# Kernel optimization log

Measured on AMD Instinct MI355X. Metric: run time of the kernel, lower is better.

## Reference

```python
import jax, jax.numpy as jnp
import numpy as np

QI8_MIN, QI8_MAX = -128.0, 127.0   # torch.qint8 iinfo
QU8_MIN, QU8_MAX = 0.0, 255.0      # torch.quint8 iinfo


def _assym_scale_offset(v, qmin, qmax):
    # mirrors get_tensor_assym_scale_offset: scale=(max-min)/(qmax-qmin), offset=qmin - min/scale
    vmin = v.min()
    vmax = v.max()
    scale = (vmax - vmin) / (qmax - qmin)
    offset = qmin - vmin / scale
    return scale, offset


def _fake_quant(v, scale, zp, qmin, qmax):
    # torch.quantize_per_tensor: q = clamp(round(v/scale + zp), qmin, qmax); dequant = (q - zp)*scale
    q = jnp.clip(jnp.round(v / scale + zp), qmin, qmax)
    return (q - zp) * scale


def setup_inputs() -> dict:
    key = jax.random.key(0)
    k1, k2, k3 = jax.random.split(key, 3)
    x = jax.random.normal(k1, (8192, 4096), jnp.float32)          # quantized activation input (modeled as float)
    weight = jax.random.normal(k2, (4096, 4096), jnp.float32) * 0.02  # Linear.weight [out, in]
    bias = jax.random.normal(k3, (4096,), jnp.float32) * 0.01
    return {"x": x, "weight": weight, "bias": bias}


def reference(x, weight, bias):
    # --- weight quantization (qint8, per-tensor asymmetric, done at __init__) ---
    w_scale, w_off = _assym_scale_offset(weight, QI8_MIN, QI8_MAX)
    w_zp = jnp.round(w_off)  # torch casts zero_point to int
    w_dq = _fake_quant(weight, w_scale, w_zp, QI8_MIN, QI8_MAX)

    # --- input is a quint8 quantized tensor; model quantize->dequantize ---
    x_scale, x_off = _assym_scale_offset(x, QU8_MIN, QU8_MAX)
    x_zp = jnp.round(x_off)
    x_dq = _fake_quant(x, x_scale, x_zp, QU8_MIN, QU8_MAX)

    # --- calibration pass (not _computed): float Linear on dequantized input ---
    act = x_dq @ weight.T + bias                 # [tokens, out]
    a_scale, a_off = _assym_scale_offset(act, QU8_MIN, QU8_MAX)
    a_zp = jnp.round(a_off)

    # --- qF.linear: int8 GEMM (dequantized form) + bias, requantized to quint8 ---
    out = x_dq @ w_dq.T + bias
    return _fake_quant(out, a_scale, a_zp, QU8_MIN, QU8_MAX)
```

## Files before the change

kernel.cpp:

```cpp
#include <hip/hip_runtime.h>
#include <stdint.h>

#define M_DIM 8192
#define N_DIM 4096
#define K_DIM 4096

typedef __attribute__((ext_vector_type(4))) int i32x4;

__device__ __forceinline__ unsigned fkey(float f) {
  unsigned u = __float_as_uint(f);
  return (u & 0x80000000u) ? ~u : (u | 0x80000000u);
}
__device__ __forceinline__ float finv(unsigned k) {
  return __uint_as_float((k & 0x80000000u) ? (k ^ 0x80000000u) : ~k);
}
__device__ __forceinline__ void async16(const void* g, void* l) {
  __builtin_amdgcn_global_load_lds(
      (const __attribute__((address_space(1))) void*)g,
      (__attribute__((address_space(3))) void*)l, 16, 0, 0);
}

__global__ void minmax_fused(const float* __restrict__ x, const float* __restrict__ w,
                             unsigned* __restrict__ stats) {
  const bool isX = blockIdx.x < 2048;
  const float4* v4 = isX ? (const float4*)x : (const float4*)w;
  const int n4 = isX ? (M_DIM * K_DIM / 4) : (N_DIM * K_DIM / 4);
  const int bid = isX ? blockIdx.x : (blockIdx.x - 2048);
  const int nb = isX ? 2048 : 1024;
  int i0 = bid * blockDim.x + threadIdx.x;
  int stride = nb * blockDim.x;
  float vmin = 3.4e38f, vmax = -3.4e38f;
  for (int i = i0; i < n4; i += stride) {
    float4 t = v4[i];
    vmin = fminf(vmin, fminf(fminf(t.x, t.y), fminf(t.z, t.w)));
    vmax = fmaxf(vmax, fmaxf(fmaxf(t.x, t.y), fmaxf(t.z, t.w)));
  }
  unsigned kmin = fkey(vmin), kmax = ~fkey(vmax);
  #pragma unroll
  for (int off = 32; off; off >>= 1) {
    unsigned t0 = __shfl_down(kmin, (unsigned)off, 64);
    unsigned t1 = __shfl_down(kmax, (unsigned)off, 64);
    kmin = kmin < t0 ? kmin : t0;
    kmax = kmax < t1 ? kmax : t1;
  }
  if ((threadIdx.x & 63) == 0) {
    int base = isX ? 0 : 2;
    atomicMin(&stats[base + 0], kmin);
    atomicMin(&stats[base + 1], kmax);
  }
}

__global__ void quant_fused(const float* __restrict__ x, const float* __restrict__ w,
                            const unsigned* __restrict__ stats,
                            signed char* __restrict__ A8, signed char* __restrict__ B8,
                            signed char* __restrict__ R8,
                            int* __restrict__ rowA, int* __restrict__ colB, int* __restrict__ colR) {
  __shared__ int sr[8];
  const int tid = threadIdx.x;
  const int lane = tid & 63;
  const int wv = tid >> 6;
  if (blockIdx.x < M_DIM) {
    const int row = blockIdx.x;
    const float xmin = finv(stats[0]), xmax = finv(~stats[1]);
    const float xs = (xmax - xmin) / 255.0f;
    const float xzp = rintf(0.0f - xmin / xs);
    const float4* xr = (const float4*)(x + (size_t)row * K_DIM);
    char4* ar = (char4*)(A8 + (size_t)row * K_DIM);
    int s = 0;
    #pragma unroll
    for (int i = 0; i < 4; ++i) {
      int idx = tid + i * 256;
      float4 t = xr[idx];
      int q0 = (int)(fminf(fmaxf(rintf(t.x / xs + xzp), 0.f), 255.f)) - 128;
      int q1 = (int)(fminf(fmaxf(rintf(t.y / xs + xzp), 0.f), 255.f)) - 128;
      int q2 = (int)(fminf(fmaxf(rintf(t.z / xs + xzp), 0.f), 255.f)) - 128;
      int q3 = (int)(fminf(fmaxf(rintf(t.w / xs + xzp), 0.f), 255.f)) - 128;
      char4 c4; c4.x = (signed char)q0; c4.y = (signed char)q1;
      c4.z = (signed char)q2; c4.w = (signed char)q3;
      ar[idx] = c4;
      s += q0 + q1 + q2 + q3;
    }
    #pragma unroll
    for (int off = 32; off; off >>= 1) s += __shfl_down(s, (unsigned)off, 64);
    if (lane == 0) sr[wv] = s;
    __syncthreads();
    if (tid == 0) rowA[row] = sr[0] + sr[1] + sr[2] + sr[3];
  } else {
    const int row = blockIdx.x - M_DIM;
    const float wmin = finv(stats[2]), wmax = finv(~stats[3]);
    const float ws = (wmax - wmin) / 255.0f;
    const float wzp = rintf(-128.0f - wmin / ws);
    const float inv_rs = 126.0f / ws;
    const float4* wr = (const float4*)(w + (size_t)row * K_DIM);
    char4* br = (char4*)(B8 + (size_t)row * K_DIM);
    char4* rr = (char4*)(R8 + (size_t)row * K_DIM);
    int sb = 0, srr = 0;
    #pragma unroll
    for (int i = 0; i < 4; ++i) {
      int idx = tid + i * 256;
      float4 t = wr[idx];
      char4 bq, rq;
      float v, qf; int q, r;
      v = t.x; qf = fminf(fmaxf(rintf(v / ws + wzp), -128.f), 127.f); q = (int)qf;
      r = (int)fminf(fmaxf(rintf((v - ws * (qf - wzp)) * inv_rs), -127.f), 127.f);
      bq.x = (signed char)q; rq.x = (signed char)r; sb += q; srr += r;
      v = t.y; qf = fminf(fmaxf(rintf(v / ws + wzp), -128.f), 127.f); q = (int)qf;
      r = (int)fminf(fmaxf(rintf((v - ws * (qf - wzp)) * inv_rs), -127.f), 127.f);
      bq.y = (signed char)q; rq.y = (signed char)r; sb += q; srr += r;
      v = t.z; qf = fminf(fmaxf(rintf(v / ws + wzp), -128.f), 127.f); q = (int)qf;
      r = (int)fminf(fmaxf(rintf((v - ws * (qf - wzp)) * inv_rs), -127.f), 127.f);
      bq.z = (signed char)q; rq.z = (signed char)r; sb += q; srr += r;
      v = t.w; qf = fminf(fmaxf(rintf(v / ws + wzp), -128.f), 127.f); q = (int)qf;
      r = (int)fminf(fmaxf(rintf((v - ws * (qf - wzp)) * inv_rs), -127.f), 127.f);
      bq.w = (signed char)q; rq.w = (signed char)r; sb += q; srr += r;
      br[idx] = bq; rr[idx] = rq;
    }
    #pragma unroll
    for (int off = 32; off; off >>= 1) {
      sb += __shfl_down(sb, (unsigned)off, 64);
      srr += __shfl_down(srr, (unsigned)off, 64);
    }
    if (lane == 0) { sr[wv] = sb; sr[4 + wv] = srr; }
    __syncthreads();
    if (tid == 0) {
      colB[row] = sr[0] + sr[1] + sr[2] + sr[3];
      colR[row] = sr[4] + sr[5] + sr[6] + sr[7];
    }
  }
}

__global__ __launch_bounds__(512, 4) void gemm_i8(
    const signed char* __restrict__ A8, const signed char* __restrict__ B8,
    const signed char* __restrict__ R8,
    const int* __restrict__ rowA, const int* __restrict__ colB, const int* __restrict__ colR,
    const float* __restrict__ bias, unsigned* __restrict__ stats,
    float* __restrict__ outp) {
  __shared__ __align__(16) signed char sA[3 * 128 * 64];
  __shared__ __align__(16) signed char sB[3 * 128 * 64];
  __shared__ __align__(16) signed char sR[3 * 128 * 64];
  __shared__ unsigned s_red[2];

  const int tid = threadIdx.x;
  const int wave = tid >> 6;
  const int lane = tid & 63;
  const int xcd = blockIdx.x & 7;
  const int s = blockIdx.x >> 3;
  const int bn = xcd * 4 + (s >> 6);
  const int bm = s & 63;
  const int rowBase = bm * 128;
  const int colBase = bn * 128;
  const int wr = wave >> 2;
  const int wc = wave & 3;
  const int laneR = lane & 15;
  const int laneK = (lane >> 4) * 16;

  if (tid == 0) { s_red[0] = 0xFFFFFFFFu; s_red[1] = 0xFFFFFFFFu; }

  i32x4 acc_q[4][2];
  i32x4 acc_r[4][2];
  const i32x4 zero = {0, 0, 0, 0};
  #pragma unroll
  for (int i = 0; i < 4; ++i) { acc_q[i][0] = zero; acc_q[i][1] = zero;
                                acc_r[i][0] = zero; acc_r[i][1] = zero; }

  const signed char* srcA = A8 + (size_t)(rowBase + wave * 16 + laneR) * K_DIM + laneK;
  const signed char* srcB = B8 + (size_t)(colBase + wave * 16 + laneR) * K_DIM + laneK;
  const signed char* srcR = R8 + (size_t)(colBase + wave * 16 + laneR) * K_DIM + laneK;
  signed char* dA = sA + wave * 1024 + lane * 16;
  signed char* dB = sB + wave * 1024 + lane * 16;
  signed char* dR = sR + wave * 1024 + lane * 16;

#define STAGE(off, kt) do {                      \
    async16(srcA + (kt), dA + (off));            \
    async16(srcB + (kt), dB + (off));            \
    async16(srcR + (kt), dR + (off));            \
  } while (0)

#define COMPUTE(off) do {                                                      \
    i32x4 af[4];                                                               \
    _Pragma("unroll")                                                          \
    for (int mi = 0; mi < 4; ++mi)                                             \
      af[mi] = *(const i32x4*)(sA + (off) + (wr * 4 + mi) * 1024 + lane * 16); \
    i32x4 bf[2], rf[2];                                                        \
    _Pragma("unroll")                                                          \
    for (int ni = 0; ni < 2; ++ni) {                                           \
      const int bo = (off) + (wc * 2 + ni) * 1024 + lane * 16;                 \
      bf[ni] = *(const i32x4*)(sB + bo);                                       \
      rf[ni] = *(const i32x4*)(sR + bo);                                       \
    }                                                                          \
    __builtin_amdgcn_s_setprio(1);                                             \
    _Pragma("unroll")                                                          \
    for (int ni = 0; ni < 2; ++ni) {                                           \
      _Pragma("unroll")                                                        \
      for (int mi = 0; mi < 4; ++mi) {                                         \
        acc_q[mi][ni] = __builtin_amdgcn_mfma_i32_16x16x64_i8(af[mi], bf[ni], acc_q[mi][ni], 0, 0, 0); \
        acc_r[mi][ni] = __builtin_amdgcn_mfma_i32_16x16x64_i8(af[mi], rf[ni], acc_r[mi][ni], 0, 0, 0); \
      }                                                                        \
    }                                                                          \
    __builtin_amdgcn_s_setprio(0);                                             \
  } while (0)

  STAGE(0, 0);
  STAGE(8192, 64);

  int o0 = 0, o1 = 8192, o2 = 16384;

  for (int t = 0; t < 62; ++t) {
    asm volatile("s_waitcnt vmcnt(3)" ::: "memory");
    __builtin_amdgcn_s_barrier();
    STAGE(o2, (t + 2) * 64);
    COMPUTE(o0);
    int tmp = o0; o0 = o1; o1 = o2; o2 = tmp;
  }
  asm volatile("s_waitcnt vmcnt(3)" ::: "memory");
  __builtin_amdgcn_s_barrier();
  COMPUTE(o0);
  { int tmp = o0; o0 = o1; o1 = o2; o2 = tmp; }
  asm volatile("s_waitcnt vmcnt(0)" ::: "memory");
  __builtin_amdgcn_s_barrier();
  COMPUTE(o0);

#undef STAGE
#undef COMPUTE

  const float xmin = finv(stats[0]), xmax = finv(~stats[1]);
  const float xs = (xmax - xmin) / 255.0f;
  const float xzp = rintf(0.0f - xmin / xs);
  const float wmin = finv(stats[2]), wmax = finv(~stats[3]);
  const float ws = (wmax - wmin) / 255.0f;
  const float wzp = rintf(-128.0f - wmin / ws);
  const int c = 128 - (int)xzp;
  const int wzpi = (int)wzp;
  const float sw = xs * ws;
  const float xrs = xs * (ws / 126.0f);
  const int ccK = c * wzpi * K_DIM;
  unsigned kmin = 0xFFFFFFFFu, kmax = 0xFFFFFFFFu;

  int rAv[4][4];
  #pragma unroll
  for (int mi = 0; mi < 4; ++mi) {
    const int row0 = rowBase + wr * 64 + mi * 16 + (lane >> 4) * 4;
    #pragma unroll
    for (int r = 0; r < 4; ++r) rAv[mi][r] = rowA[row0 + r];
  }

  #pragma unroll
  for (int ni = 0; ni < 2; ++ni) {
    const int col = colBase + wc * 32 + ni * 16 + laneR;
    const float bv = bias[col];
    const int base_n = c * colB[col] - ccK;
    const int cR = c * colR[col];
    #pragma unroll
    for (int mi = 0; mi < 4; ++mi) {
      const int row0 = rowBase + wr * 64 + mi * 16 + (lane >> 4) * 4;
      #pragma unroll
      for (int r = 0; r < 4; ++r) {
        const int S = acc_q[mi][ni][r] + base_n - wzpi * rAv[mi][r];
        const float ov = sw * (float)S + bv;
        const int S2 = acc_r[mi][ni][r] + cR;
        const float av = ov + xrs * (float)S2;
        const unsigned k = fkey(av);
        const unsigned kf = ~k;
        kmin = kmin < k ? kmin : k;
        kmax = kmax < kf ? kmax : kf;
        outp[(size_t)(row0 + r) * N_DIM + col] = ov;
      }
    }
  }

  #pragma unroll
  for (int off = 32; off; off >>= 1) {
    unsigned t0 = __shfl_down(kmin, (unsigned)off, 64);
    unsigned t1 = __shfl_down(kmax, (unsigned)off, 64);
    kmin = kmin < t0 ? kmin : t0;
    kmax = kmax < t1 ? kmax : t1;
  }
  __syncthreads();
  if (lane == 0) { atomicMin(&s_red[0], kmin); atomicMin(&s_red[1], kmax); }
  __syncthreads();
  if (tid == 0) { atomicMin(&stats[4], s_red[0]); atomicMin(&stats[5], s_red[1]); }
}

__global__ void requant_kernel(float* __restrict__ out, const unsigned* __restrict__ stats, int n4) {
  const float amin = finv(stats[4]), amax = finv(~stats[5]);
  const float as = (amax - amin) / 255.0f;
  const float azp = rintf(0.0f - amin / as);
  float4* o4 = (float4*)out;
  int i0 = blockIdx.x * blockDim.x + threadIdx.x;
  int stride = gridDim.x * blockDim.x;
  for (int i = i0; i < n4; i += stride) {
    float4 t = o4[i];
    t.x = (fminf(fmaxf(rintf(t.x / as + azp), 0.f), 255.f) - azp) * as;
    t.y = (fminf(fmaxf(rintf(t.y / as + azp), 0.f), 255.f) - azp) * as;
    t.z = (fminf(fmaxf(rintf(t.z / as + azp), 0.f), 255.f) - azp) * as;
    t.w = (fminf(fmaxf(rintf(t.w / as + azp), 0.f), 255.f) - azp) * as;
    o4[i] = t;
  }
}

extern "C" void kernel_launch(void* const* d_in, const int* in_sizes, int n_in,
                              void* d_out, int out_size, void* d_ws, size_t ws_size,
                              hipStream_t stream) {
  const float* x = (const float*)d_in[0];
  const float* w = (const float*)d_in[1];
  const float* bias = (const float*)d_in[2];
  float* out = (float*)d_out;

  unsigned* stats = (unsigned*)d_ws;
  signed char* A8 = (signed char*)d_ws + 256;
  signed char* B8 = A8 + (size_t)M_DIM * K_DIM;
  signed char* R8 = B8 + (size_t)N_DIM * K_DIM;
  int* rowA = (int*)(R8 + (size_t)N_DIM * K_DIM);
  int* colB = rowA + M_DIM;
  int* colR = colB + N_DIM;

  hipMemsetAsync(stats, 0xFF, 24, stream);
  minmax_fused<<<3072, 256, 0, stream>>>(x, w, stats);
  quant_fused<<<M_DIM + N_DIM, 256, 0, stream>>>(x, w, stats, A8, B8, R8, rowA, colB, colR);
  gemm_i8<<<(M_DIM / 128) * (N_DIM / 128), 512, 0, stream>>>(A8, B8, R8, rowA, colB, colR, bias, stats, out);
  requant_kernel<<<2048, 256, 0, stream>>>(out, stats, M_DIM * N_DIM / 4);
}
```

Measured before the change: 965.2 us.

## Fuse min/max and quantization into one cooperative kernel; unroll GEMM pipeline by three

Merges the min/max reduction and quantization kernels into a single cooperative kernel of 1024 blocks that uses a grid-wide sync between the phases. This removes one launch and its gap. Each block now quantizes 8 activation rows and 4 weight rows, which adds grid-sync cost and lowers parallelism. The GEMM main loop is also unrolled by three with constant LDS buffer offsets, so the buffer-rotation registers and index arithmetic go away.

Measured after the change: 958.1 us. Within noise of the previous version (-0.7%).

```diff
diff --git a/kernel.cpp b/kernel.cpp
--- a/kernel.cpp
+++ b/kernel.cpp
@@ -1,5 +1,8 @@
 #include <hip/hip_runtime.h>
+#include <hip/hip_cooperative_groups.h>
 #include <stdint.h>
+
+namespace cg = cooperative_groups;
 
 #define M_DIM 8192
 #define N_DIM 4096
@@ -20,111 +23,126 @@
       (__attribute__((address_space(3))) void*)l, 16, 0, 0);
 }
 
-__global__ void minmax_fused(const float* __restrict__ x, const float* __restrict__ w,
-                             unsigned* __restrict__ stats) {
-  const bool isX = blockIdx.x < 2048;
-  const float4* v4 = isX ? (const float4*)x : (const float4*)w;
-  const int n4 = isX ? (M_DIM * K_DIM / 4) : (N_DIM * K_DIM / 4);
-  const int bid = isX ? blockIdx.x : (blockIdx.x - 2048);
-  const int nb = isX ? 2048 : 1024;
-  int i0 = bid * blockDim.x + threadIdx.x;
-  int stride = nb * blockDim.x;
-  float vmin = 3.4e38f, vmax = -3.4e38f;
-  for (int i = i0; i < n4; i += stride) {
-    float4 t = v4[i];
-    vmin = fminf(vmin, fminf(fminf(t.x, t.y), fminf(t.z, t.w)));
-    vmax = fmaxf(vmax, fmaxf(fmaxf(t.x, t.y), fmaxf(t.z, t.w)));
-  }
-  unsigned kmin = fkey(vmin), kmax = ~fkey(vmax);
-  #pragma unroll
-  for (int off = 32; off; off >>= 1) {
-    unsigned t0 = __shfl_down(kmin, (unsigned)off, 64);
-    unsigned t1 = __shfl_down(kmax, (unsigned)off, 64);
-    kmin = kmin < t0 ? kmin : t0;
-    kmax = kmax < t1 ? kmax : t1;
-  }
-  if ((threadIdx.x & 63) == 0) {
-    int base = isX ? 0 : 2;
-    atomicMin(&stats[base + 0], kmin);
-    atomicMin(&stats[base + 1], kmax);
-  }
-}
-
-__global__ void quant_fused(const float* __restrict__ x, const float* __restrict__ w,
-                            const unsigned* __restrict__ stats,
-                            signed char* __restrict__ A8, signed char* __restrict__ B8,
-                            signed char* __restrict__ R8,
-                            int* __restrict__ rowA, int* __restrict__ colB, int* __restrict__ colR) {
+__global__ __launch_bounds__(256, 4) void minmax_quant(
+    const float* __restrict__ x, const float* __restrict__ w,
+    unsigned* __restrict__ stats,
+    signed char* __restrict__ A8, signed char* __restrict__ B8,
+    signed char* __restrict__ R8,
+    int* __restrict__ rowA, int* __restrict__ colB, int* __restrict__ colR) {
   __shared__ int sr[8];
   const int tid = threadIdx.x;
   const int lane = tid & 63;
   const int wv = tid >> 6;
-  if (blockIdx.x < M_DIM) {
-    const int row = blockIdx.x;
-    const float xmin = finv(stats[0]), xmax = finv(~stats[1]);
-    const float xs = (xmax - xmin) / 255.0f;
-    const float xzp = rintf(0.0f - xmin / xs);
-    const float4* xr = (const float4*)(x + (size_t)row * K_DIM);
-    char4* ar = (char4*)(A8 + (size_t)row * K_DIM);
-    int s = 0;
-    #pragma unroll
-    for (int i = 0; i < 4; ++i) {
-      int idx = tid + i * 256;
-      float4 t = xr[idx];
-      int q0 = (int)(fminf(fmaxf(rintf(t.x / xs + xzp), 0.f), 255.f)) - 128;
-      int q1 = (int)(fminf(fmaxf(rintf(t.y / xs + xzp), 0.f), 255.f)) - 128;
-      int q2 = (int)(fminf(fmaxf(rintf(t.z / xs + xzp), 0.f), 255.f)) - 128;
-      int q3 = (int)(fminf(fmaxf(rintf(t.w / xs + xzp), 0.f), 255.f)) - 128;
-      char4 c4; c4.x = (signed char)q0; c4.y = (signed char)q1;
-      c4.z = (signed char)q2; c4.w = (signed char)q3;
-      ar[idx] = c4;
-      s += q0 + q1 + q2 + q3;
-    }
-    #pragma unroll
-    for (int off = 32; off; off >>= 1) s += __shfl_down(s, (unsigned)off, 64);
-    if (lane == 0) sr[wv] = s;
-    __syncthreads();
-    if (tid == 0) rowA[row] = sr[0] + sr[1] + sr[2] + sr[3];
-  } else {
-    const int row = blockIdx.x - M_DIM;
-    const float wmin = finv(stats[2]), wmax = finv(~stats[3]);
-    const float ws = (wmax - wmin) / 255.0f;
-    const float wzp = rintf(-128.0f - wmin / ws);
-    const float inv_rs = 126.0f / ws;
-    const float4* wr = (const float4*)(w + (size_t)row * K_DIM);
-    char4* br = (char4*)(B8 + (size_t)row * K_DIM);
-    char4* rr = (char4*)(R8 + (size_t)row * K_DIM);
-    int sb = 0, srr = 0;
-    #pragma unroll
-    for (int i = 0; i < 4; ++i) {
-      int idx = tid + i * 256;
-      float4 t = wr[idx];
-      char4 bq, rq;
-      float v, qf; int q, r;
-      v = t.x; qf = fminf(fmaxf(rintf(v / ws + wzp), -128.f), 127.f); q = (int)qf;
-      r = (int)fminf(fmaxf(rintf((v - ws * (qf - wzp)) * inv_rs), -127.f), 127.f);
-      bq.x = (signed char)q; rq.x = (signed char)r; sb += q; srr += r;
-      v = t.y; qf = fminf(fmaxf(rintf(v / ws + wzp), -128.f), 127.f); q = (int)qf;
-      r = (int)fminf(fmaxf(rintf((v - ws * (qf - wzp)) * inv_rs), -127.f), 127.f);
-      bq.y = (signed char)q; rq.y = (signed char)r; sb += q; srr += r;
-      v = t.z; qf = fminf(fmaxf(rintf(v / ws + wzp), -128.f), 127.f); q = (int)qf;
-      r = (int)fminf(fmaxf(rintf((v - ws * (qf - wzp)) * inv_rs), -127.f), 127.f);
-      bq.z = (signed char)q; rq.z = (signed char)r; sb += q; srr += r;
-      v = t.w; qf = fminf(fmaxf(rintf(v / ws + wzp), -128.f), 127.f); q = (int)qf;
-      r = (int)fminf(fmaxf(rintf((v - ws * (qf - wzp)) * inv_rs), -127.f), 127.f);
-      bq.w = (signed char)q; rq.w = (signed char)r; sb += q; srr += r;
-      br[idx] = bq; rr[idx] = rq;
-    }
+
+  {
+    const float4* x4 = (const float4*)x;
+    const float4* w4 = (const float4*)w;
+    const int n4x = M_DIM * K_DIM / 4;
+    const int n4w = N_DIM * K_DIM / 4;
+    const int i0 = blockIdx.x * 256 + tid;
+    const int stride = 1024 * 256;
+    float xmn = 3.4e38f, xmx = -3.4e38f, wmn = 3.4e38f, wmx = -3.4e38f;
+    for (int i = i0; i < n4x; i += stride) {
+      float4 t = x4[i];
+      xmn = fminf(xmn, fminf(fminf(t.x, t.y), fminf(t.z, t.w)));
+      xmx = fmaxf(xmx, fmaxf(fmaxf(t.x, t.y), fmaxf(t.z, t.w)));
+    }
+    for (int i = i0; i < n4w; i += stride) {
+      float4 t = w4[i];
+      wmn = fminf(wmn, fminf(fminf(t.x, t.y), fminf(t.z, t.w)));
+      wmx = fmaxf(wmx, fmaxf(fmaxf(t.x, t.y), fmaxf(t.z, t.w)));
+    }
+    unsigned k0 = fkey(xmn), k1 = ~fkey(xmx), k2 = fkey(wmn), k3 = ~fkey(wmx);
     #pragma unroll
     for (int off = 32; off; off >>= 1) {
-      sb += __shfl_down(sb, (unsigned)off, 64);
-      srr += __shfl_down(srr, (unsigned)off, 64);
-    }
-    if (lane == 0) { sr[wv] = sb; sr[4 + wv] = srr; }
-    __syncthreads();
-    if (tid == 0) {
-      colB[row] = sr[0] + sr[1] + sr[2] + sr[3];
-      colR[row] = sr[4] + sr[5] + sr[6] + sr[7];
+      unsigned t0 = __shfl_down(k0, (unsigned)off, 64);
+      unsigned t1 = __shfl_down(k1, (unsigned)off, 64);
+      unsigned t2 = __shfl_down(k2, (unsigned)off, 64);
+      unsigned t3 = __shfl_down(k3, (unsigned)off, 64);
+      k0 = k0 < t0 ? k0 : t0;  k1 = k1 < t1 ? k1 : t1;
+      k2 = k2 < t2 ? k2 : t2;  k3 = k3 < t3 ? k3 : t3;
+    }
+    if (lane == 0) {
+      atomicMin(&stats[0], k0);
+      atomicMin(&stats[1], k1);
+      atomicMin(&stats[2], k2);
+      atomicMin(&stats[3], k3);
+    }
+  }
+
+  cg::this_grid().sync();
+
+  const float xmin = finv(stats[0]), xmax = finv(~stats[1]);
+  const float xs = (xmax - xmin) / 255.0f;
+  const float xzp = rintf(0.0f - xmin / xs);
+  const float wmin = finv(stats[2]), wmax = finv(~stats[3]);
+  const float ws = (wmax - wmin) / 255.0f;
+  const float wzp = rintf(-128.0f - wmin / ws);
+  const float inv_rs = 126.0f / ws;
+
+  for (int r = 0; r < 12; ++r) {
+    if (r < 8) {
+      const int row = blockIdx.x + r * 1024;
+      const float4* xr = (const float4*)(x + (size_t)row * K_DIM);
+      char4* ar = (char4*)(A8 + (size_t)row * K_DIM);
+      int s = 0;
+      #pragma unroll
+      for (int i = 0; i < 4; ++i) {
+        int idx = tid + i * 256;
+        float4 t = xr[idx];
+        int q0 = (int)(fminf(fmaxf(rintf(t.x / xs + xzp), 0.f), 255.f)) - 128;
+        int q1 = (int)(fminf(fmaxf(rintf(t.y / xs + xzp), 0.f), 255.f)) - 128;
+        int q2 = (int)(fminf(fmaxf(rintf(t.z / xs + xzp), 0.f), 255.f)) - 128;
+        int q3 = (int)(fminf(fmaxf(rintf(t.w / xs + xzp), 0.f), 255.f)) - 128;
+        char4 c4; c4.x = (signed char)q0; c4.y = (signed char)q1;
+        c4.z = (signed char)q2; c4.w = (signed char)q3;
+        ar[idx] = c4;
+        s += q0 + q1 + q2 + q3;
+      }
+      #pragma unroll
+      for (int off = 32; off; off >>= 1) s += __shfl_down(s, (unsigned)off, 64);
+      if (lane == 0) sr[wv] = s;
+      __syncthreads();
+      if (tid == 0) rowA[row] = sr[0] + sr[1] + sr[2] + sr[3];
+      __syncthreads();
+    } else {
+      const int row = blockIdx.x + (r - 8) * 1024;
+      const float4* wr = (const float4*)(w + (size_t)row * K_DIM);
+      char4* br = (char4*)(B8 + (size_t)row * K_DIM);
+      char4* rr = (char4*)(R8 + (size_t)row * K_DIM);
+      int sb = 0, srr = 0;
+      #pragma unroll
+      for (int i = 0; i < 4; ++i) {
+        int idx = tid + i * 256;
+        float4 t = wr[idx];
+        char4 bq, rq;
+        float v, qf; int q, rv;
+        v = t.x; qf = fminf(fmaxf(rintf(v / ws + wzp), -128.f), 127.f); q = (int)qf;
+        rv = (int)fminf(fmaxf(rintf((v - ws * (qf - wzp)) * inv_rs), -127.f), 127.f);
+        bq.x = (signed char)q; rq.x = (signed char)rv; sb += q; srr += rv;
+        v = t.y; qf = fminf(fmaxf(rintf(v / ws + wzp), -128.f), 127.f); q = (int)qf;
+        rv = (int)fminf(fmaxf(rintf((v - ws * (qf - wzp)) * inv_rs), -127.f), 127.f);
+        bq.y = (signed char)q; rq.y = (signed char)rv; sb += q; srr += rv;
+        v = t.z; qf = fminf(fmaxf(rintf(v / ws + wzp), -128.f), 127.f); q = (int)qf;
+        rv = (int)fminf(fmaxf(rintf((v - ws * (qf - wzp)) * inv_rs), -127.f), 127.f);
+        bq.z = (signed char)q; rq.z = (signed char)rv; sb += q; srr += rv;
+        v = t.w; qf = fminf(fmaxf(rintf(v / ws + wzp), -128.f), 127.f); q = (int)qf;
+        rv = (int)fminf(fmaxf(rintf((v - ws * (qf - wzp)) * inv_rs), -127.f), 127.f);
+        bq.w = (signed char)q; rq.w = (signed char)rv; sb += q; srr += rv;
+        br[idx] = bq; rr[idx] = rq;
+      }
+      #pragma unroll
+      for (int off = 32; off; off >>= 1) {
+        sb += __shfl_down(sb, (unsigned)off, 64);
+        srr += __shfl_down(srr, (unsigned)off, 64);
+      }
+      if (lane == 0) { sr[wv] = sb; sr[4 + wv] = srr; }
+      __syncthreads();
+      if (tid == 0) {
+        colB[row] = sr[0] + sr[1] + sr[2] + sr[3];
+        colR[row] = sr[4] + sr[5] + sr[6] + sr[7];
+      }
+      __syncthreads();
     }
   }
 }
@@ -163,28 +181,28 @@
   for (int i = 0; i < 4; ++i) { acc_q[i][0] = zero; acc_q[i][1] = zero;
                                 acc_r[i][0] = zero; acc_r[i][1] = zero; }
 
-  const signed char* srcA = A8 + (size_t)(rowBase + wave * 16 + laneR) * K_DIM + laneK;
-  const signed char* srcB = B8 + (size_t)(colBase + wave * 16 + laneR) * K_DIM + laneK;
-  const signed char* srcR = R8 + (size_t)(colBase + wave * 16 + laneR) * K_DIM + laneK;
+  const signed char* pA = A8 + (size_t)(rowBase + wave * 16 + laneR) * K_DIM + laneK;
+  const signed char* pB = B8 + (size_t)(colBase + wave * 16 + laneR) * K_DIM + laneK;
+  const signed char* pR = R8 + (size_t)(colBase + wave * 16 + laneR) * K_DIM + laneK;
   signed char* dA = sA + wave * 1024 + lane * 16;
   signed char* dB = sB + wave * 1024 + lane * 16;
   signed char* dR = sR + wave * 1024 + lane * 16;
 
-#define STAGE(off, kt) do {                      \
-    async16(srcA + (kt), dA + (off));            \
-    async16(srcB + (kt), dB + (off));            \
-    async16(srcR + (kt), dR + (off));            \
+#define STAGE(SO, GO) do {                       \
+    async16(pA + (GO), dA + (SO));               \
+    async16(pB + (GO), dB + (SO));               \
+    async16(pR + (GO), dR + (SO));               \
   } while (0)
 
-#define COMPUTE(off) do {                                                      \
+#define COMPUTE(OFF) do {                                                      \
     i32x4 af[4];                                                               \
     _Pragma("unroll")                                                          \
     for (int mi = 0; mi < 4; ++mi)                                             \
-      af[mi] = *(const i32x4*)(sA + (off) + (wr * 4 + mi) * 1024 + lane * 16); \
+      af[mi] = *(const i32x4*)(sA + (OFF) + (wr * 4 + mi) * 1024 + lane * 16); \
     i32x4 bf[2], rf[2];                                                        \
     _Pragma("unroll")                                                          \
     for (int ni = 0; ni < 2; ++ni) {                                           \
-      const int bo = (off) + (wc * 2 + ni) * 1024 + lane * 16;                 \
+      const int bo = (OFF) + (wc * 2 + ni) * 1024 + lane * 16;                 \
       bf[ni] = *(const i32x4*)(sB + bo);                                       \
       rf[ni] = *(const i32x4*)(sR + bo);                                       \
     }                                                                          \
@@ -200,26 +218,32 @@
     __builtin_amdgcn_s_setprio(0);                                             \
   } while (0)
 
+#define STEP(CO, SO, GO) do {                            \
+    asm volatile("s_waitcnt vmcnt(3)" ::: "memory");     \
+    __builtin_amdgcn_s_barrier();                        \
+    STAGE(SO, GO);                                       \
+    COMPUTE(CO);                                         \
+  } while (0)
+
   STAGE(0, 0);
   STAGE(8192, 64);
 
-  int o0 = 0, o1 = 8192, o2 = 16384;
-
-  for (int t = 0; t < 62; ++t) {
-    asm volatile("s_waitcnt vmcnt(3)" ::: "memory");
-    __builtin_amdgcn_s_barrier();
-    STAGE(o2, (t + 2) * 64);
-    COMPUTE(o0);
-    int tmp = o0; o0 = o1; o1 = o2; o2 = tmp;
-  }
+  for (int t3 = 0; t3 < 20; ++t3) {
+    STEP(0,     16384, 128);
+    STEP(8192,  0,     192);
+    STEP(16384, 8192,  256);
+    pA += 192; pB += 192; pR += 192;
+  }
+  STEP(0,    16384, 128);
+  STEP(8192, 0,     192);
   asm volatile("s_waitcnt vmcnt(3)" ::: "memory");
   __builtin_amdgcn_s_barrier();
-  COMPUTE(o0);
-  { int tmp = o0; o0 = o1; o1 = o2; o2 = tmp; }
+  COMPUTE(16384);
   asm volatile("s_waitcnt vmcnt(0)" ::: "memory");
   __builtin_amdgcn_s_barrier();
-  COMPUTE(o0);
-
+  COMPUTE(0);
+
+#undef STEP
 #undef STAGE
 #undef COMPUTE
 
@@ -315,8 +339,11 @@
   int* colR = colB + N_DIM;
 
   hipMemsetAsync(stats, 0xFF, 24, stream);
-  minmax_fused<<<3072, 256, 0, stream>>>(x, w, stats);
-  quant_fused<<<M_DIM + N_DIM, 256, 0, stream>>>(x, w, stats, A8, B8, R8, rowA, colB, colR);
+
+  void* kargs[] = {(void*)&x, (void*)&w, (void*)&stats, (void*)&A8, (void*)&B8,
+                   (void*)&R8, (void*)&rowA, (void*)&colB, (void*)&colR};
+  hipLaunchCooperativeKernel((void*)minmax_quant, dim3(1024), dim3(256), kargs, 0, stream);
+
   gemm_i8<<<(M_DIM / 128) * (N_DIM / 128), 512, 0, stream>>>(A8, B8, R8, rowA, colB, colR, bias, stats, out);
   requant_kernel<<<2048, 256, 0, stream>>>(out, stats, M_DIM * N_DIM / 4);
 }
```
